# Kernel optimization log

Measured on AMD Instinct MI355X. Metric: run time of the kernel, lower is better.

The kernel has to match this reference:

```python
import jax, jax.numpy as jnp
import numpy as np

B, C, H, W = 8, 64, 112, 112
O, K, PAD, STRIDE = 64, 3, 1, 1
KK = K * K
OH = (H - K + 2 * PAD) // STRIDE + 1
OW = (W - K + 2 * PAD) // STRIDE + 1
L = OH * OW  # number of patches


def setup_inputs() -> dict:
    key = jax.random.key(0)
    k1, k2, k3 = jax.random.split(key, 3)
    x = jax.random.normal(k1, (B, C, H, W), dtype=jnp.float32)
    weight = jax.random.normal(k2, (O, C, K, K), dtype=jnp.float32)
    # one uniformly random kernel position to zero out, per patch (nums=1)
    mask_idx = jax.random.randint(k3, (L,), 0, KK, dtype=jnp.int32)
    return {"x": x, "weight": weight, "mask_idx": mask_idx}


def reference(x, weight, mask_idx):
    b = x.shape[0]
    # im2col: [b, C*KK, OH, OW], feature dim ordered channel-major (c, kh, kw)
    # which matches torch.nn.Unfold ordering.
    patches = jax.lax.conv_general_dilated_patches(
        x, (K, K), (STRIDE, STRIDE), ((PAD, PAD), (PAD, PAD)))
    patches = patches.reshape(b, C * KK, L)  # [b, CK, L]

    # Per-patch mask over kernel positions, tiled across channels
    # (equivalent to mask.repeat(1, in_channels) in the original).
    mask = jnp.ones((L, KK), dtype=x.dtype).at[jnp.arange(L), mask_idx].set(0.0)
    mask_full = jnp.tile(mask, (1, C))  # [L, C*KK]

    # weight.view(O, -1).t() -> [CK, O]; masking the weight rows per patch is
    # mathematically identical to masking the unfolded input per patch, which
    # avoids materializing the [L, CK, O] masked weight tensor.
    w2 = weight.reshape(O, C * KK).T  # [CK, O]
    out = jnp.einsum('bkl,lk,ko->bol', patches, mask_full, w2)  # [b, O, L]
    return out.reshape(b, O, OH, OW)
```

## Files before the change

### kernel.cpp

```cpp
#include <hip/hip_runtime.h>
#include <hip/hip_bf16.h>
#include <cstdint>

#define Bn 8
#define Cn 64
#define Hn 112
#define Wn 112
#define On 64
#define Ln (Hn * Wn)
#define HP 114
#define WP 114

typedef __attribute__((ext_vector_type(4)))  float f32x4;
typedef __attribute__((ext_vector_type(16))) float f32x16;
typedef __attribute__((ext_vector_type(8)))  short bf16x8;
typedef __attribute__((ext_vector_type(4)))  unsigned int u32x4;

__device__ __forceinline__ unsigned f2bf(float f) {
    unsigned u = __float_as_uint(f);
    unsigned r = 0x7fffu + ((u >> 16) & 1u);
    return (u + r) >> 16;
}

__global__ __launch_bounds__(64) void wpack_kernel(const float* __restrict__ w,
                                                   unsigned short* __restrict__ wpk) {
    int idx = blockIdx.x;
    int kc = idx & 3, wr = (idx >> 2) & 1, p = idx >> 3;
    int lane = threadIdx.x;
    int o  = wr * 32 + (lane & 31);
    int cb = kc * 16 + (lane >> 5) * 8;
    unsigned pk[4];
#pragma unroll
    for (int j = 0; j < 4; j++) {
        float v0 = w[((size_t)o * Cn + cb + 2 * j) * 9 + p];
        float v1 = w[((size_t)o * Cn + cb + 2 * j + 1) * 9 + p];
        pk[j] = f2bf(v0) | (f2bf(v1) << 16);
    }
    u32x4 v; v[0] = pk[0]; v[1] = pk[1]; v[2] = pk[2]; v[3] = pk[3];
    reinterpret_cast<u32x4*>(wpk)[idx * 64 + lane] = v;
}

__global__ __launch_bounds__(256, 2) void conv_fused(const float* __restrict__ x,
                                                     const unsigned short* __restrict__ wpk,
                                                     const int* __restrict__ mask_idx,
                                                     float* __restrict__ out) {
    __shared__ char xs[4 * WP * Cn * 2];

    int b  = blockIdx.x & 7;
    int lt = blockIdx.x >> 3;
    int l0 = lt * 128;
    int oh0 = l0 / Wn;

    int tid  = threadIdx.x;
    int wave = tid >> 6, lane = tid & 63;
    int hi = lane >> 5;
    int li = lane & 31;

    int lg = l0 + wave * 32 + li;
    int oh = lg / Wn, ow = lg - oh * Wn;
    int r  = oh - oh0;
    int mv = mask_idx[lg];

    const float* xb = x + (size_t)b * Cn * Hn * Wn;
#pragma unroll
    for (int it = 0; it < 15; ++it) {
        int q = tid + it * 256;
        if (q < 4 * 8 * WP) {
            int row = q / (8 * WP);
            int rem = q - row * (8 * WP);
            int c8  = rem / WP;
            int wp  = rem - c8 * WP;
            int h = oh0 + row - 1;
            int w = wp - 1;
            bool inb = ((unsigned)h < (unsigned)Hn) & ((unsigned)w < (unsigned)Wn);
            const float* s = xb + ((size_t)(c8 * 8) * Hn + (inb ? h : 0)) * Wn + (inb ? w : 0);
            unsigned pk[4];
#pragma unroll
            for (int j = 0; j < 4; ++j) {
                float v0 = s[(size_t)(2 * j)     * (Hn * Wn)];
                float v1 = s[(size_t)(2 * j + 1) * (Hn * Wn)];
                if (!inb) { v0 = 0.f; v1 = 0.f; }
                pk[j] = f2bf(v0) | (f2bf(v1) << 16);
            }
            int qs = (row * WP + wp) * 8 + c8;
            int off = (qs * 16) ^ ((wp & 7) << 4);
            u32x4 v; v[0] = pk[0]; v[1] = pk[1]; v[2] = pk[2]; v[3] = pk[3];
            *reinterpret_cast<u32x4*>(xs + off) = v;
        }
    }

    const u32x4* wv = reinterpret_cast<const u32x4*>(wpk);
    u32x4 af0[8], af1[8];
#pragma unroll
    for (int f = 0; f < 8; ++f) af0[f] = wv[f * 64 + lane];

    f32x16 acc0 = {}, acc1 = {};
    const u32x4 vzero = {0u, 0u, 0u, 0u};

    __syncthreads();

#pragma unroll
    for (int p = 0; p < 9; ++p) {
        u32x4* cur = (p & 1) ? af1 : af0;
        u32x4* nxt = (p & 1) ? af0 : af1;
        if (p < 8) {
#pragma unroll
            for (int f = 0; f < 8; ++f)
                nxt[f] = wv[((p + 1) * 8 + f) * 64 + lane];
        }

        int dh = p / 3, dw = p - dh * 3;
        int wq   = ow + dw;
        int base = ((r + dh) * WP + wq) << 7;
        int swz  = (wq & 7) << 4;
        u32x4 bv[4];
#pragma unroll
        for (int kc = 0; kc < 4; ++kc) {
            int off = (base + ((2 * kc + hi) << 4)) ^ swz;
            bv[kc] = *reinterpret_cast<const u32x4*>(xs + off);
        }
        if (mv == p) { bv[0] = vzero; bv[1] = vzero; bv[2] = vzero; bv[3] = vzero; }

#pragma unroll
        for (int kc = 0; kc < 4; ++kc) {
            bf16x8 bb = *reinterpret_cast<bf16x8*>(&bv[kc]);
            bf16x8 a0 = *reinterpret_cast<bf16x8*>(&cur[kc]);
            bf16x8 a1 = *reinterpret_cast<bf16x8*>(&cur[4 + kc]);
            acc0 = __builtin_amdgcn_mfma_f32_32x32x16_bf16(a0, bb, acc0, 0, 0, 0);
            acc1 = __builtin_amdgcn_mfma_f32_32x32x16_bf16(a1, bb, acc1, 0, 0, 0);
        }
    }

    float* ob = out + (size_t)(b * On) * Ln + lg;
#pragma unroll
    for (int reg = 0; reg < 16; ++reg) {
        int orow = (reg & 3) + 8 * (reg >> 2) + 4 * hi;
        ob[(size_t)orow * Ln]        = acc0[reg];
        ob[(size_t)(orow + 32) * Ln] = acc1[reg];
    }
}

extern "C" void kernel_launch(void* const* d_in, const int* in_sizes, int n_in,
                              void* d_out, int out_size, void* d_ws, size_t ws_size,
                              hipStream_t stream) {
    const float* x    = (const float*)d_in[0];
    const float* w    = (const float*)d_in[1];
    const int*   mask = (const int*)d_in[2];
    float* out = (float*)d_out;

    unsigned short* wpk = (unsigned short*)d_ws;

    wpack_kernel<<<72,      64,  0, stream>>>(w, wpk);
    conv_fused  <<<Bn * 98, 256, 0, stream>>>(x, wpk, mask, out);
}
```

Measured before the change: 98.06 us.

## Pre-pack padded bf16 NHWC input in prep kernel; read conv tiles directly from global

A separate prep kernel now converts the whole input to a zero-padded bf16 channels-last buffer in workspace, alongside the weight packing. The conv kernel drops its shared-memory staging and barrier and loads its B fragments straight from that buffer through L2/cache. Occupancy hints go from 2 to 4 blocks per CU. This removes the redundant per-block fp32 gather and halo re-conversion but adds a full extra round trip of the input through memory and relies on cache hits for the nine overlapping tap reads.

```diff
diff --git a/kernel.cpp b/kernel.cpp
--- a/kernel.cpp
+++ b/kernel.cpp
@@ -22,34 +22,63 @@
     return (u + r) >> 16;
 }
 
-__global__ __launch_bounds__(64) void wpack_kernel(const float* __restrict__ w,
+__global__ __launch_bounds__(128) void prep_kernel(const float* __restrict__ x,
+                                                   const float* __restrict__ w,
+                                                   unsigned short* __restrict__ xps,
                                                    unsigned short* __restrict__ wpk) {
-    int idx = blockIdx.x;
-    int kc = idx & 3, wr = (idx >> 2) & 1, p = idx >> 3;
-    int lane = threadIdx.x;
-    int o  = wr * 32 + (lane & 31);
-    int cb = kc * 16 + (lane >> 5) * 8;
-    unsigned pk[4];
+    int blk = blockIdx.x;
+    int t = threadIdx.x;
+    if (blk < 912) {
+        int b = blk / HP, row = blk - b * HP;
+        int c8  = t >> 4;
+        int wpl = t & 15;
+        int h = row - 1;
+        const float* xb = x + (size_t)b * Cn * Hn * Wn;
+        unsigned short* dst = xps + ((size_t)(b * HP + row) * WP) * Cn;
 #pragma unroll
-    for (int j = 0; j < 4; j++) {
-        float v0 = w[((size_t)o * Cn + cb + 2 * j) * 9 + p];
-        float v1 = w[((size_t)o * Cn + cb + 2 * j + 1) * 9 + p];
-        pk[j] = f2bf(v0) | (f2bf(v1) << 16);
+        for (int g = 0; g < 8; ++g) {
+            int wp = wpl + (g << 4);
+            if (wp < WP) {
+                int wcol = wp - 1;
+                bool inb = ((unsigned)h < (unsigned)Hn) & ((unsigned)wcol < (unsigned)Wn);
+                const float* s = xb + ((size_t)(c8 * 8) * Hn + (inb ? h : 0)) * Wn + (inb ? wcol : 0);
+                unsigned pk[4];
+#pragma unroll
+                for (int j = 0; j < 4; ++j) {
+                    float v0 = s[(size_t)(2 * j)     * (Hn * Wn)];
+                    float v1 = s[(size_t)(2 * j + 1) * (Hn * Wn)];
+                    if (!inb) { v0 = 0.f; v1 = 0.f; }
+                    pk[j] = f2bf(v0) | (f2bf(v1) << 16);
+                }
+                u32x4 v; v[0] = pk[0]; v[1] = pk[1]; v[2] = pk[2]; v[3] = pk[3];
+                *reinterpret_cast<u32x4*>(dst + (size_t)wp * Cn + c8 * 8) = v;
+            }
+        }
+    } else {
+        int idx = (blk - 912) * 2 + (t >> 6);
+        int lane = t & 63;
+        int kc = idx & 3, wr2 = (idx >> 2) & 1, p = idx >> 3;
+        int o  = wr2 * 32 + (lane & 31);
+        int cb = kc * 16 + (lane >> 5) * 8;
+        unsigned pk[4];
+#pragma unroll
+        for (int j = 0; j < 4; ++j) {
+            float v0 = w[((size_t)o * Cn + cb + 2 * j) * 9 + p];
+            float v1 = w[((size_t)o * Cn + cb + 2 * j + 1) * 9 + p];
+            pk[j] = f2bf(v0) | (f2bf(v1) << 16);
+        }
+        u32x4 v; v[0] = pk[0]; v[1] = pk[1]; v[2] = pk[2]; v[3] = pk[3];
+        reinterpret_cast<u32x4*>(wpk)[idx * 64 + lane] = v;
     }
-    u32x4 v; v[0] = pk[0]; v[1] = pk[1]; v[2] = pk[2]; v[3] = pk[3];
-    reinterpret_cast<u32x4*>(wpk)[idx * 64 + lane] = v;
 }
 
-__global__ __launch_bounds__(256, 2) void conv_fused(const float* __restrict__ x,
-                                                     const unsigned short* __restrict__ wpk,
-                                                     const int* __restrict__ mask_idx,
-                                                     float* __restrict__ out) {
-    __shared__ char xs[4 * WP * Cn * 2];
-
+__global__ __launch_bounds__(256, 4) void conv_direct(const unsigned short* __restrict__ xps,
+                                                      const unsigned short* __restrict__ wpk,
+                                                      const int* __restrict__ mask_idx,
+                                                      float* __restrict__ out) {
     int b  = blockIdx.x & 7;
     int lt = blockIdx.x >> 3;
     int l0 = lt * 128;
-    int oh0 = l0 / Wn;
 
     int tid  = threadIdx.x;
     int wave = tid >> 6, lane = tid & 63;
@@ -58,46 +87,19 @@
 
     int lg = l0 + wave * 32 + li;
     int oh = lg / Wn, ow = lg - oh * Wn;
-    int r  = oh - oh0;
     int mv = mask_idx[lg];
 
-    const float* xb = x + (size_t)b * Cn * Hn * Wn;
-#pragma unroll
-    for (int it = 0; it < 15; ++it) {
-        int q = tid + it * 256;
-        if (q < 4 * 8 * WP) {
-            int row = q / (8 * WP);
-            int rem = q - row * (8 * WP);
-            int c8  = rem / WP;
-            int wp  = rem - c8 * WP;
-            int h = oh0 + row - 1;
-            int w = wp - 1;
-            bool inb = ((unsigned)h < (unsigned)Hn) & ((unsigned)w < (unsigned)Wn);
-            const float* s = xb + ((size_t)(c8 * 8) * Hn + (inb ? h : 0)) * Wn + (inb ? w : 0);
-            unsigned pk[4];
-#pragma unroll
-            for (int j = 0; j < 4; ++j) {
-                float v0 = s[(size_t)(2 * j)     * (Hn * Wn)];
-                float v1 = s[(size_t)(2 * j + 1) * (Hn * Wn)];
-                if (!inb) { v0 = 0.f; v1 = 0.f; }
-                pk[j] = f2bf(v0) | (f2bf(v1) << 16);
-            }
-            int qs = (row * WP + wp) * 8 + c8;
-            int off = (qs * 16) ^ ((wp & 7) << 4);
-            u32x4 v; v[0] = pk[0]; v[1] = pk[1]; v[2] = pk[2]; v[3] = pk[3];
-            *reinterpret_cast<u32x4*>(xs + off) = v;
-        }
-    }
+    const char* xb = (const char*)(xps + ((size_t)(b * HP + oh) * WP + ow) * Cn)
+                   + hi * 16;
 
     const u32x4* wv = reinterpret_cast<const u32x4*>(wpk);
+    const u32x4 vzero = {0u, 0u, 0u, 0u};
+
     u32x4 af0[8], af1[8];
 #pragma unroll
     for (int f = 0; f < 8; ++f) af0[f] = wv[f * 64 + lane];
 
     f32x16 acc0 = {}, acc1 = {};
-    const u32x4 vzero = {0u, 0u, 0u, 0u};
-
-    __syncthreads();
 
 #pragma unroll
     for (int p = 0; p < 9; ++p) {
@@ -110,15 +112,11 @@
         }
 
         int dh = p / 3, dw = p - dh * 3;
-        int wq   = ow + dw;
-        int base = ((r + dh) * WP + wq) << 7;
-        int swz  = (wq & 7) << 4;
+        const char* bp = xb + (dh * WP + dw) * (Cn * 2);
         u32x4 bv[4];
 #pragma unroll
-        for (int kc = 0; kc < 4; ++kc) {
-            int off = (base + ((2 * kc + hi) << 4)) ^ swz;
-            bv[kc] = *reinterpret_cast<const u32x4*>(xs + off);
-        }
+        for (int kc = 0; kc < 4; ++kc)
+            bv[kc] = *reinterpret_cast<const u32x4*>(bp + kc * 32);
         if (mv == p) { bv[0] = vzero; bv[1] = vzero; bv[2] = vzero; bv[3] = vzero; }
 
 #pragma unroll
@@ -148,8 +146,9 @@
     const int*   mask = (const int*)d_in[2];
     float* out = (float*)d_out;
 
-    unsigned short* wpk = (unsigned short*)d_ws;
+    unsigned short* xps = (unsigned short*)d_ws;
+    unsigned short* wpk = (unsigned short*)((char*)d_ws + 13307904);
 
-    wpack_kernel<<<72,      64,  0, stream>>>(w, wpk);
-    conv_fused  <<<Bn * 98, 256, 0, stream>>>(x, wpk, mask, out);
+    prep_kernel<<<948,     128, 0, stream>>>(x, w, xps, wpk);
+    conv_direct<<<Bn * 98, 256, 0, stream>>>(xps, wpk, mask, out);
 }
```

Measured after the change: 113.3 us. 1.15x slower.
